# Kernel tuning notes

Measured on AMD Instinct MI355X. Metric: run time of the kernel, lower is better.

## Reference

```python
import jax, jax.numpy as jnp
import numpy as np
from jax import lax

D_MODEL = 1024
D_STATE = 16
D_CONV = 4
EXPAND = 2
D_INNER = D_MODEL * EXPAND
BATCH = 2
SEQLEN = 2048


def setup_inputs() -> dict:
    key = jax.random.key(0)
    ks = jax.random.split(key, 8)
    sc = lambda k, shape, s: jax.random.normal(k, shape, dtype=jnp.float32) * s
    x = jax.random.normal(ks[0], (BATCH, SEQLEN, D_MODEL), dtype=jnp.float32)
    W_in = sc(ks[1], (D_MODEL, 2 * D_INNER), 0.02)          # in_proj (no bias)
    conv_w = sc(ks[2], (D_INNER, 1, D_CONV), 0.1)            # depthwise conv kernel (O, I/g, K)
    conv_b = jnp.zeros((D_INNER,), jnp.float32)
    W_param = sc(ks[3], (D_INNER, 1 + 2 * D_STATE), 0.02)    # param_proj (no bias)
    w_dt = sc(ks[4], (D_INNER,), 0.1)                        # dt_proj weight (d_inner, 1) flattened
    b_dt = jnp.zeros((D_INNER,), jnp.float32)
    A_log = jnp.log(jnp.tile(jnp.arange(1, D_STATE + 1, dtype=jnp.float32), (D_INNER, 1)))
    D_param = jnp.ones((D_INNER,), jnp.float32)
    W_out = sc(ks[5], (D_INNER, D_MODEL), 0.02)              # out_proj (no bias)
    return {"x": x, "W_in": W_in, "conv_w": conv_w, "conv_b": conv_b,
            "W_param": W_param, "w_dt": w_dt, "b_dt": b_dt,
            "A_log": A_log, "D_param": D_param, "W_out": W_out}


def _silu(v):
    return v * jax.nn.sigmoid(v)


def _forward(x, W_in, conv_w, conv_b, W_param, w_dt, b_dt, A_log, D_param, W_out):
    # input projection -> two branches
    xz = x @ W_in                                   # (B, S, 2*d_inner)
    x_branch, z_branch = jnp.split(xz, 2, axis=-1)
    # depthwise causal conv1d (torch pads k-1 both sides then slices [:seqlen] == left pad k-1)
    xc = lax.conv_general_dilated(
        x_branch.transpose(0, 2, 1), conv_w,
        window_strides=(1,), padding=[(D_CONV - 1, 0)],
        feature_group_count=D_INNER,
        dimension_numbers=("NCH", "OIH", "NCH"))
    x_branch = _silu((xc + conv_b[None, :, None]).transpose(0, 2, 1))  # (B, S, d_inner)
    # SSM parameters
    params = x_branch @ W_param                     # (B, S, 1+2n)
    dt_raw = params[..., :1]                        # (B, S, 1)
    B_mat = params[..., 1:1 + D_STATE]              # (B, S, n)
    C_mat = params[..., 1 + D_STATE:]               # (B, S, n)
    dt = jax.nn.softplus(dt_raw * w_dt + b_dt)      # (B, S, d_inner)
    A = -jnp.exp(A_log)                             # (d_inner, n)

    def step(h, inp):
        x_t, dt_t, B_t, C_t = inp                   # (B,i),(B,i),(B,n),(B,n)
        A_bar = jnp.exp(A * dt_t[..., None])        # (B, i, n)
        h = A_bar * h + (dt_t[..., None] * B_t[:, None, :]) * x_t[..., None]
        y_t = jnp.einsum('bin,bn->bi', h, C_t)
        return h, y_t

    h0 = jnp.zeros((x.shape[0], D_INNER, D_STATE), x.dtype)
    xs = (x_branch.transpose(1, 0, 2), dt.transpose(1, 0, 2),
          B_mat.transpose(1, 0, 2), C_mat.transpose(1, 0, 2))
    _, ys = lax.scan(step, h0, xs)                  # ys: (S, B, d_inner)
    y = ys.transpose(1, 0, 2) + D_param * x_branch
    y = y * _silu(z_branch)
    return y @ W_out                                # (B, S, d_model)


def reference(x, W_in, conv_w, conv_b, W_param, w_dt, b_dt, A_log, D_param, W_out):
    return _forward(x, W_in, conv_w, conv_b, W_param, w_dt, b_dt, A_log, D_param, W_out)
```

## Files before the change

### kernel.cpp

```cpp
#include <hip/hip_runtime.h>

typedef unsigned int uint;
typedef unsigned short ushort;

using f32x4  = __attribute__((ext_vector_type(4))) float;
using bf16x8 = __attribute__((ext_vector_type(8))) short;

#define LOG2E 1.44269504f
#define LN2   0.69314718f

__device__ __forceinline__ float fexp2(float x) { return __builtin_amdgcn_exp2f(x); }
__device__ __forceinline__ float flog2(float x) { return __builtin_amdgcn_logf(x); }
__device__ __forceinline__ float frcp (float x) { return __builtin_amdgcn_rcpf(x); }
__device__ __forceinline__ float fsilu(float x) {
  return x * frcp(1.f + fexp2(-LOG2E * x));
}
__device__ __forceinline__ float fsoftplus(float u) {
  float e = fexp2(u * LOG2E);
  float l = LN2 * flog2(1.f + e);
  return (u > 20.f) ? u : l;
}

__device__ __forceinline__ ushort f2b(float f) {
  uint u = __builtin_bit_cast(uint, f);
  u = (u + 0x7fffu + ((u >> 16) & 1u)) >> 16;
  return (ushort)u;
}
__device__ __forceinline__ float b2f(ushort h) {
  return __builtin_bit_cast(float, (uint)h << 16);
}

__device__ __forceinline__ void gload_lds16(const void* g, void* l) {
  __builtin_amdgcn_global_load_lds(
      (const __attribute__((address_space(1))) uint*)g,
      (__attribute__((address_space(3))) uint*)l, 16, 0, 0);
}

#define SBAR  asm volatile("s_barrier" ::: "memory")
#define LG0   do { asm volatile("s_waitcnt lgkmcnt(0)" ::: "memory"); \
                   __builtin_amdgcn_sched_barrier(0); } while (0)
#define VMW(n) do { asm volatile("s_waitcnt vmcnt(" #n ")" ::: "memory"); \
                    __builtin_amdgcn_sched_barrier(0); } while (0)

__global__ __launch_bounds__(256) void cvt_bf16(const float* __restrict__ in,
                                                ushort* __restrict__ out) {
  const int idx = blockIdx.x * 256 + threadIdx.x;
  const float4 v = *(const float4*)&in[(size_t)idx << 2];
  ushort4 o = { f2b(v.x), f2b(v.y), f2b(v.z), f2b(v.w) };
  *(ushort4*)&out[(size_t)idx << 2] = o;
}

__global__ __launch_bounds__(256) void transpose_cvt(const float* __restrict__ in,
                                                     ushort* __restrict__ out,
                                                     int R, int C) {
  __shared__ float tile[32][33];
  const int c0 = blockIdx.x << 5, r0 = blockIdx.y << 5;
  const int tx = threadIdx.x, ty = threadIdx.y;
  for (int j = ty; j < 32; j += 8)
    tile[j][tx] = in[(size_t)(r0 + j) * C + c0 + tx];
  __syncthreads();
  for (int j = ty; j < 32; j += 8)
    out[(size_t)(c0 + j) * R + r0 + tx] = f2b(tile[tx][j]);
}

__global__ __launch_bounds__(256) void wprep(const float* __restrict__ Wp,
                                             ushort* __restrict__ whi,
                                             ushort* __restrict__ wlo) {
  const int idx = blockIdx.x * 256 + threadIdx.x;
  const int n = idx >> 11, k = idx & 2047;
  float v = (n < 33) ? Wp[k * 33 + n] : 0.f;
  ushort h = f2b(v);
  whi[idx] = h;
  wlo[idx] = f2b(v - b2f(h));
}

__device__ __forceinline__ void ldfA(bf16x8 (&a)[8], const ushort* base,
                                     int wq, int lane) {
  const int fr = lane & 15;
  const int ce = (((lane >> 4) ^ (fr & 7)) << 3);
  #pragma unroll
  for (int mi = 0; mi < 4; ++mi) {
    const ushort* p = base + (wq + mi * 16 + fr) * 64;
    a[mi * 2 + 0] = *(const bf16x8*)(p + ce);
    a[mi * 2 + 1] = *(const bf16x8*)(p + (ce ^ 32));
  }
}
__device__ __forceinline__ void ldfB(bf16x8 (&b)[4], const ushort* base,
                                     int wq, int lane) {
  const int fr = lane & 15;
  const int ce = (((lane >> 4) ^ (fr & 7)) << 3);
  #pragma unroll
  for (int ni = 0; ni < 2; ++ni) {
    const ushort* p = base + (wq + ni * 16 + fr) * 64;
    b[ni * 2 + 0] = *(const bf16x8*)(p + ce);
    b[ni * 2 + 1] = *(const bf16x8*)(p + (ce ^ 32));
  }
}
__device__ __forceinline__ void mfma16(f32x4 (&acc)[8][4], const bf16x8 (&a)[8],
                                       const bf16x8 (&b)[4], int qm, int qn) {
  #pragma unroll
  for (int mi = 0; mi < 4; ++mi)
    #pragma unroll
    for (int ni = 0; ni < 2; ++ni)
      #pragma unroll
      for (int s = 0; s < 2; ++s)
        acc[qm * 4 + mi][qn * 2 + ni] = __builtin_amdgcn_mfma_f32_16x16x32_bf16(
            a[mi * 2 + s], b[ni * 2 + s], acc[qm * 4 + mi][qn * 2 + ni], 0, 0, 0);
}

__global__ __launch_bounds__(512, 2) void gemm_bf16_8ph(
    const ushort* __restrict__ A, const ushort* __restrict__ Bt,
    float* __restrict__ C, int M, int N, int K, int lgx) {
  __shared__ __align__(16) ushort lds[65536];
  const int tid = threadIdx.x;
  int w = blockIdx.x;
  const int chunk = (int)(gridDim.x >> 3);
  w = (w & 7) * chunk + (w >> 3);
  const int m0 = (w >> lgx) << 8;
  const int n0 = (w & ((1 << lgx) - 1)) << 8;
  const int lane = tid & 63, wid = tid >> 6;
  const int wm = wid >> 2, wn = wid & 3;
  const int srow = tid >> 3;
  const int scol = (((tid & 7) ^ (srow & 7)) << 3);
  const int swave = wid << 9;

  auto stA = [&](int t, int h) {
    const ushort* g = A + (size_t)(m0 + h * 128 + srow) * K + (t << 6) + scol;
    ushort* l = lds + ((t & 1) << 14) + (h << 13) + swave;
    gload_lds16(g, l);
    gload_lds16(g + (size_t)64 * K, l + 4096);
  };
  auto stB = [&](int t, int h) {
    const ushort* g = Bt + (size_t)(n0 + h * 128 + srow) * K + (t << 6) + scol;
    ushort* l = lds + 32768 + ((t & 1) << 14) + (h << 13) + swave;
    gload_lds16(g, l);
    gload_lds16(g + (size_t)64 * K, l + 4096);
  };

  f32x4 acc[8][4] = {};
  const int niter = K >> 7;

  stA(0, 0); stB(0, 0); stA(0, 1); stB(0, 1); stA(1, 0);
  VMW(2);
  SBAR;

  for (int it = 0; it < niter; ++it) {
    const int E = it << 1, O = E | 1;
    const bool pred = (it < niter - 1);
    const ushort* A0 = lds;
    const ushort* B0 = lds + 32768;
    const ushort* A1 = lds + 16384;
    const ushort* B1 = lds + 49152;
    bf16x8 a[8], b0[4], b1[4];
    ldfA(a, A0, wm * 128, lane);
    ldfB(b0, B0, wn * 64, lane);
    stB(O, 0);
    SBAR; LG0;
    __builtin_amdgcn_s_setprio(1); mfma16(acc, a, b0, 0, 0);
    __builtin_amdgcn_sched_barrier(0); __builtin_amdgcn_s_setprio(0);
    SBAR;
    ldfB(b1, B0, wn * 64 + 32, lane);
    stA(O, 1);
    SBAR; LG0;
    __builtin_amdgcn_s_setprio(1); mfma16(acc, a, b1, 0, 1);
    __builtin_amdgcn_sched_barrier(0); __builtin_amdgcn_s_setprio(0);
    SBAR;
    ldfA(a, A0, wm * 128 + 64, lane);
    stB(O, 1);
    SBAR; LG0;
    __builtin_amdgcn_s_setprio(1); mfma16(acc, a, b0, 1, 0);
    __builtin_amdgcn_sched_barrier(0); __builtin_amdgcn_s_setprio(0);
    SBAR;
    if (pred) stA(E + 2, 0);
    SBAR; LG0;
    __builtin_amdgcn_s_setprio(1); mfma16(acc, a, b1, 1, 1);
    __builtin_amdgcn_sched_barrier(0); __builtin_amdgcn_s_setprio(0);
    if (pred) { VMW(2); } else { VMW(0); }
    SBAR;
    ldfA(a, A1, wm * 128, lane);
    ldfB(b0, B1, wn * 64, lane);
    if (pred) stB(E + 2, 0);
    SBAR; LG0;
    __builtin_amdgcn_s_setprio(1); mfma16(acc, a, b0, 0, 0);
    __builtin_amdgcn_sched_barrier(0); __builtin_amdgcn_s_setprio(0);
    SBAR;
    ldfB(b1, B1, wn * 64 + 32, lane);
    if (pred) stA(E + 2, 1);
    SBAR; LG0;
    __builtin_amdgcn_s_setprio(1); mfma16(acc, a, b1, 0, 1);
    __builtin_amdgcn_sched_barrier(0); __builtin_amdgcn_s_setprio(0);
    SBAR;
    ldfA(a, A1, wm * 128 + 64, lane);
    if (pred) stB(E + 2, 1);
    SBAR; LG0;
    __builtin_amdgcn_s_setprio(1); mfma16(acc, a, b0, 1, 0);
    __builtin_amdgcn_sched_barrier(0); __builtin_amdgcn_s_setprio(0);
    SBAR;
    if (pred) stA(O + 2, 0);
    SBAR; LG0;
    __builtin_amdgcn_s_setprio(1); mfma16(acc, a, b1, 1, 1);
    __builtin_amdgcn_sched_barrier(0); __builtin_amdgcn_s_setprio(0);
    VMW(2);
    SBAR;
  }

  const int rbase = m0 + wm * 128 + ((lane >> 4) << 2);
  const int cbase = n0 + wn * 64 + (lane & 15);
  #pragma unroll
  for (int mi = 0; mi < 8; ++mi)
    #pragma unroll
    for (int ni = 0; ni < 4; ++ni)
      #pragma unroll
      for (int r = 0; r < 4; ++r)
        C[(size_t)(rbase + mi * 16 + r) * N + cbase + ni * 16] = acc[mi][ni][r];
}

__global__ __launch_bounds__(256) void gemm_bf16(const ushort* __restrict__ A,
                                                 const ushort* __restrict__ Bt,
                                                 float* __restrict__ C,
                                                 int M, int N, int K, int lgx) {
  __shared__ __align__(16) ushort As[128 * 64];
  __shared__ __align__(16) ushort Bs[128 * 64];
  const int tid  = threadIdx.x;
  int w = (blockIdx.y << lgx) + blockIdx.x;
  const int chunk = (int)((gridDim.x * gridDim.y) >> 3);
  w = (w & 7) * chunk + (w >> 3);
  const int m0 = (w >> lgx) << 7, n0 = (w & ((1 << lgx) - 1)) << 7;
  const int lane = tid & 63, wid = tid >> 6;
  const int wm   = wid >> 1, wn = wid & 1;
  const int fr   = lane & 15;
  const int kg   = (lane >> 4) << 3;
  const int g_row = tid >> 3;
  const int g_col = (tid & 7) << 3;
  f32x4 acc[4][4] = {};
  for (int k0 = 0; k0 < K; k0 += 64) {
    __syncthreads();
    const ushort* gA = A  + (size_t)(m0 + g_row) * K + k0 + g_col;
    const ushort* gB = Bt + (size_t)(n0 + g_row) * K + k0 + g_col;
    #pragma unroll
    for (int j = 0; j < 4; ++j) {
      gload_lds16(gA + (size_t)(j * 32) * K, As + j * 2048 + wid * 512);
      gload_lds16(gB + (size_t)(j * 32) * K, Bs + j * 2048 + wid * 512);
    }
    __syncthreads();
    #pragma unroll
    for (int ks = 0; ks < 64; ks += 32) {
      bf16x8 a[4], b[4];
      #pragma unroll
      for (int m = 0; m < 4; ++m)
        a[m] = *(const bf16x8*)(As + (wm * 64 + m * 16 + fr) * 64 + ks + kg);
      #pragma unroll
      for (int n = 0; n < 4; ++n)
        b[n] = *(const bf16x8*)(Bs + (wn * 64 + n * 16 + fr) * 64 + ks + kg);
      #pragma unroll
      for (int m = 0; m < 4; ++m)
        #pragma unroll
        for (int n = 0; n < 4; ++n)
          acc[m][n] = __builtin_amdgcn_mfma_f32_16x16x32_bf16(a[m], b[n], acc[m][n], 0, 0, 0);
    }
  }
  const int rbase = m0 + wm * 64 + ((lane >> 4) << 2);
  const int cbase = n0 + wn * 64 + fr;
  #pragma unroll
  for (int sm = 0; sm < 4; ++sm)
    #pragma unroll
    for (int sn = 0; sn < 4; ++sn)
      #pragma unroll
      for (int r = 0; r < 4; ++r)
        C[(size_t)(rbase + sm * 16 + r) * N + cbase + sn * 16] = acc[sm][sn][r];
}

__global__ __launch_bounds__(256) void params_mfma(const ushort* __restrict__ xhi,
                                                   const ushort* __restrict__ xlo,
                                                   const ushort* __restrict__ whi,
                                                   const ushort* __restrict__ wlo,
                                                   float* __restrict__ xz) {
  __shared__ __align__(16) ushort Ah[128 * 64], Al[128 * 64];
  __shared__ __align__(16) ushort Bh[64 * 64],  Bl[64 * 64];
  const int mt = blockIdx.x >> 2, ks = blockIdx.x & 3;
  const int m0 = mt << 7;
  const int k00 = ks << 9;
  const int tid = threadIdx.x, lane = tid & 63, wid = tid >> 6;
  const int fr = lane & 15, kg = (lane >> 4) << 3;
  const int g_row = tid >> 3, g_col = (tid & 7) << 3;
  f32x4 acc[2][4] = {};
  for (int k0 = k00; k0 < k00 + 512; k0 += 64) {
    __syncthreads();
    const ushort* gAh = xhi + (size_t)(m0 + g_row) * 2048 + k0 + g_col;
    const ushort* gAl = xlo + (size_t)(m0 + g_row) * 2048 + k0 + g_col;
    #pragma unroll
    for (int j = 0; j < 4; ++j) {
      gload_lds16(gAh + (size_t)(j * 32) * 2048, Ah + j * 2048 + wid * 512);
      gload_lds16(gAl + (size_t)(j * 32) * 2048, Al + j * 2048 + wid * 512);
    }
    const ushort* gWh = whi + (size_t)g_row * 2048 + k0 + g_col;
    const ushort* gWl = wlo + (size_t)g_row * 2048 + k0 + g_col;
    gload_lds16(gWh, Bh + wid * 512);
    gload_lds16(gWh + (size_t)32 * 2048, Bh + 2048 + wid * 512);
    gload_lds16(gWl, Bl + wid * 512);
    gload_lds16(gWl + (size_t)32 * 2048, Bl + 2048 + wid * 512);
    __syncthreads();
    #pragma unroll
    for (int kss = 0; kss < 64; kss += 32) {
      bf16x8 ah[2], al[2], bh[4], bl[4];
      #pragma unroll
      for (int m = 0; m < 2; ++m) {
        ah[m] = *(const bf16x8*)(Ah + (wid * 32 + m * 16 + fr) * 64 + kss + kg);
        al[m] = *(const bf16x8*)(Al + (wid * 32 + m * 16 + fr) * 64 + kss + kg);
      }
      #pragma unroll
      for (int n = 0; n < 4; ++n) {
        bh[n] = *(const bf16x8*)(Bh + (n * 16 + fr) * 64 + kss + kg);
        bl[n] = *(const bf16x8*)(Bl + (n * 16 + fr) * 64 + kss + kg);
      }
      #pragma unroll
      for (int m = 0; m < 2; ++m)
        #pragma unroll
        for (int n = 0; n < 4; ++n) {
          acc[m][n] = __builtin_amdgcn_mfma_f32_16x16x32_bf16(ah[m], bh[n], acc[m][n], 0, 0, 0);
          acc[m][n] = __builtin_amdgcn_mfma_f32_16x16x32_bf16(ah[m], bl[n], acc[m][n], 0, 0, 0);
          acc[m][n] = __builtin_amdgcn_mfma_f32_16x16x32_bf16(al[m], bh[n], acc[m][n], 0, 0, 0);
        }
    }
  }
  const int rbase = m0 + wid * 32 + ((lane >> 4) << 2);
  #pragma unroll
  for (int m = 0; m < 2; ++m)
    #pragma unroll
    for (int n = 0; n < 4; ++n)
      #pragma unroll
      for (int r = 0; r < 4; ++r)
        xz[(size_t)(rbase + m * 16 + r) * 4096 + (ks << 6) + n * 16 + fr] = acc[m][n][r];
}

__global__ __launch_bounds__(256) void conv_silu(const float* __restrict__ xz,
                                                 const float* __restrict__ cw,
                                                 const float* __restrict__ cb,
                                                 float* __restrict__ xs,
                                                 ushort* __restrict__ xhi,
                                                 ushort* __restrict__ xlo) {
  const int idx = blockIdx.x * 256 + threadIdx.x;
  const int c4  = (idx & 511) << 2;
  const int row = idx >> 9;
  const int t   = row & 2047;
  float acc[4], w0[4], w1[4], w2[4], w3[4];
  *(float4*)acc = *(const float4*)&cb[c4];
  *(float4*)w0 = *(const float4*)&cw[(c4 + 0) << 2];
  *(float4*)w1 = *(const float4*)&cw[(c4 + 1) << 2];
  *(float4*)w2 = *(const float4*)&cw[(c4 + 2) << 2];
  *(float4*)w3 = *(const float4*)&cw[(c4 + 3) << 2];
  #pragma unroll
  for (int k = 0; k < 4; ++k) {
    if (t - 3 + k >= 0) {
      const float4 v = *(const float4*)&xz[(size_t)(row - 3 + k) * 4096 + c4];
      acc[0] = fmaf(w0[k], v.x, acc[0]);
      acc[1] = fmaf(w1[k], v.y, acc[1]);
      acc[2] = fmaf(w2[k], v.z, acc[2]);
      acc[3] = fmaf(w3[k], v.w, acc[3]);
    }
  }
  float o[4];
  ushort hi[4], lo[4];
  #pragma unroll
  for (int j = 0; j < 4; ++j) {
    o[j]  = fsilu(acc[j]);
    hi[j] = f2b(o[j]);
    lo[j] = f2b(o[j] - b2f(hi[j]));
  }
  *(float4*) &xs [(size_t)idx << 2] = *(float4*)o;
  *(ushort4*)&xhi[(size_t)idx << 2] = *(ushort4*)hi;
  *(ushort4*)&xlo[(size_t)idx << 2] = *(ushort4*)lo;
}

__global__ __launch_bounds__(256) void scan_pass1(const float* __restrict__ xs,
                                                  const float* __restrict__ xz,
                                                  const float* __restrict__ w_dt,
                                                  const float* __restrict__ b_dt,
                                                  const float* __restrict__ A_log,
                                                  float2* __restrict__ sums) {
  const int blk = blockIdx.x;
  const int c   = blk & 63, bg = blk >> 6;
  const int b   = bg >> 3, cg = bg & 7;
  const int tid = threadIdx.x;
  const int i   = (cg << 8) + tid;
  __shared__ float bc_l[32][32];
  __shared__ float dtr_l[32];
  const size_t row0 = (size_t)b * 2048 + c * 32;
  for (int idx = tid; idx < 1024; idx += 256) {
    int t = idx >> 5, n = idx & 31;
    const float* p = xz + (row0 + t) * 4096 + 1 + n;
    bc_l[t][n] = (p[0] + p[64]) + (p[128] + p[192]);
  }
  if (tid < 32) {
    const float* p = xz + (row0 + tid) * 4096;
    dtr_l[tid] = (p[0] + p[64]) + (p[128] + p[192]);
  }
  const float w = w_dt[i], bb = b_dt[i];
  float An2[16];
  {
    const float4* al = (const float4*)&A_log[(size_t)i * 16];
    #pragma unroll
    for (int q = 0; q < 4; ++q) {
      float4 v = al[q];
      An2[4 * q + 0] = -fexp2(v.x * LOG2E) * LOG2E;
      An2[4 * q + 1] = -fexp2(v.y * LOG2E) * LOG2E;
      An2[4 * q + 2] = -fexp2(v.z * LOG2E) * LOG2E;
      An2[4 * q + 3] = -fexp2(v.w * LOG2E) * LOG2E;
    }
  }
  float h[16] = {};
  float dts = 0.f;
  __syncthreads();
  const float* xcol = xs + row0 * 2048 + i;
  #pragma unroll 4
  for (int t = 0; t < 32; ++t) {
    float dt = fsoftplus(fmaf(dtr_l[t], w, bb));
    dts += dt;
    float dtx = dt * xcol[(size_t)t * 2048];
    const f32x4* bp = (const f32x4*)&bc_l[t][0];
    #pragma unroll
    for (int q = 0; q < 4; ++q) {
      f32x4 Bv = bp[q];
      #pragma unroll
      for (int j = 0; j < 4; ++j) {
        const int n = 4 * q + j;
        float Ab = fexp2(An2[n] * dt);
        h[n] = fmaf(Ab, h[n], dtx * Bv[j]);
      }
    }
  }
  float4* sp = (float4*)(sums + ((size_t)(b * 64 + c) << 15) + (size_t)i * 16);
  #pragma unroll
  for (int q = 0; q < 8; ++q)
    sp[q] = make_float4(fexp2(An2[2 * q] * dts), h[2 * q],
                        fexp2(An2[2 * q + 1] * dts), h[2 * q + 1]);
}

__global__ __launch_bounds__(256) void scan_mid(float2* __restrict__ sums) {
  const int g = blockIdx.x * 256 + threadIdx.x;
  const int b = g >> 15, r = g & 32767;
  float2* base = sums + ((size_t)b << 21) + r;
  float h = 0.f;
  #pragma unroll
  for (int cb = 0; cb < 64; cb += 16) {
    float2 s[16];
    #pragma unroll
    for (int j = 0; j < 16; ++j) s[j] = base[(size_t)(cb + j) << 15];
    #pragma unroll
    for (int j = 0; j < 16; ++j) {
      base[(size_t)(cb + j) << 15].x = h;
      h = fmaf(s[j].x, h, s[j].y);
    }
  }
}

__global__ __launch_bounds__(256) void scan_pass2(const float* __restrict__ xs,
                                                  const float* __restrict__ xz,
                                                  const float* __restrict__ w_dt,
                                                  const float* __restrict__ b_dt,
                                                  const float* __restrict__ A_log,
                                                  const float* __restrict__ D_param,
                                                  const float2* __restrict__ sums,
                                                  ushort* __restrict__ yg) {
  const int blk = blockIdx.x;
  const int c   = blk & 63, bg = blk >> 6;
  const int b   = bg >> 3, cg = bg & 7;
  const int tid = threadIdx.x;
  const int i   = (cg << 8) + tid;
  __shared__ float bc_l[32][32];
  __shared__ float dtr_l[32];
  const size_t row0 = (size_t)b * 2048 + c * 32;
  for (int idx = tid; idx < 1024; idx += 256) {
    int t = idx >> 5, n = idx & 31;
    const float* p = xz + (row0 + t) * 4096 + 1 + n;
    bc_l[t][n] = (p[0] + p[64]) + (p[128] + p[192]);
  }
  if (tid < 32) {
    const float* p = xz + (row0 + tid) * 4096;
    dtr_l[tid] = (p[0] + p[64]) + (p[128] + p[192]);
  }
  const float w = w_dt[i], bb = b_dt[i];
  const float Dp = D_param[i];
  float An2[16];
  {
    const float4* al = (const float4*)&A_log[(size_t)i * 16];
    #pragma unroll
    for (int q = 0; q < 4; ++q) {
      float4 v = al[q];
      An2[4 * q + 0] = -fexp2(v.x * LOG2E) * LOG2E;
      An2[4 * q + 1] = -fexp2(v.y * LOG2E) * LOG2E;
      An2[4 * q + 2] = -fexp2(v.z * LOG2E) * LOG2E;
      An2[4 * q + 3] = -fexp2(v.w * LOG2E) * LOG2E;
    }
  }
  float h[16];
  {
    const float4* sp = (const float4*)(sums + ((size_t)(b * 64 + c) << 15) + (size_t)i * 16);
    #pragma unroll
    for (int q = 0; q < 8; ++q) {
      float4 v = sp[q];
      h[2 * q]     = v.x;
      h[2 * q + 1] = v.z;
    }
  }
  __syncthreads();
  const float*  xcol = xs + row0 * 2048 + i;
  const float*  zcol = xz + row0 * 4096 + 2048 + i;
  ushort*       ocol = yg + row0 * 2048 + i;
  #pragma unroll 4
  for (int t = 0; t < 32; ++t) {
    float dt = fsoftplus(fmaf(dtr_l[t], w, bb));
    float xv = xcol[(size_t)t * 2048];
    float dtx = dt * xv;
    float y = Dp * xv;
    const f32x4* bp = (const f32x4*)&bc_l[t][0];
    const f32x4* cp = (const f32x4*)&bc_l[t][16];
    #pragma unroll
    for (int q = 0; q < 4; ++q) {
      f32x4 Bv = bp[q], Cv = cp[q];
      #pragma unroll
      for (int j = 0; j < 4; ++j) {
        const int n = 4 * q + j;
        float Ab = fexp2(An2[n] * dt);
        h[n] = fmaf(Ab, h[n], dtx * Bv[j]);
        y = fmaf(h[n], Cv[j], y);
      }
    }
    float z = zcol[(size_t)t * 4096];
    ocol[(size_t)t * 2048] = f2b(y * fsilu(z));
  }
}

extern "C" void kernel_launch(void* const* d_in, const int* in_sizes, int n_in,
                              void* d_out, int out_size, void* d_ws, size_t ws_size,
                              hipStream_t stream) {
  const float* x       = (const float*)d_in[0];
  const float* W_in    = (const float*)d_in[1];
  const float* conv_w  = (const float*)d_in[2];
  const float* conv_b  = (const float*)d_in[3];
  const float* W_param = (const float*)d_in[4];
  const float* w_dt    = (const float*)d_in[5];
  const float* b_dt    = (const float*)d_in[6];
  const float* A_log   = (const float*)d_in[7];
  const float* D_param = (const float*)d_in[8];
  const float* W_out   = (const float*)d_in[9];
  float* out = (float*)d_out;

  char* ws = (char*)d_ws;
  float*  xz     = (float*) (ws);
  float*  x_s    = (float*) (ws + 67108864);
  ushort* WpT_hi = (ushort*)(ws + 100663296);
  ushort* WpT_lo = (ushort*)(ws + 100925440);
  float2* sums   = (float2*)(ws + 101203968);
  ushort* x_hi   = (ushort*)(ws + 101203968);
  ushort* x_lo   = (ushort*)(ws + 117981184);
  ushort* WoutT  = (ushort*)(ws + 134758400);
  ushort* yg     = (ushort*)(ws + 138952704);
  ushort* xA     = (ushort*)(ws + 155729920);
  ushort* WinT   = (ushort*)(ws + 164118528);

  cvt_bf16<<<4096, 256, 0, stream>>>(x, xA);
  transpose_cvt<<<dim3(128, 32), dim3(32, 8), 0, stream>>>(W_in,  WinT,  1024, 4096);
  transpose_cvt<<<dim3(32, 64),  dim3(32, 8), 0, stream>>>(W_out, WoutT, 2048, 1024);
  wprep<<<512, 256, 0, stream>>>(W_param, WpT_hi, WpT_lo);
  gemm_bf16_8ph<<<256, 512, 0, stream>>>(xA, WinT, xz, 4096, 4096, 1024, 4);
  conv_silu<<<8192, 256, 0, stream>>>(xz, conv_w, conv_b, x_s, x_hi, x_lo);
  params_mfma<<<128, 256, 0, stream>>>(x_hi, x_lo, WpT_hi, WpT_lo, xz);
  scan_pass1<<<1024, 256, 0, stream>>>(x_s, xz, w_dt, b_dt, A_log, sums);
  scan_mid<<<256, 256, 0, stream>>>(sums);
  scan_pass2<<<1024, 256, 0, stream>>>(x_s, xz, w_dt, b_dt, A_log, D_param, sums, yg);
  gemm_bf16<<<dim3(8, 32), 256, 0, stream>>>(yg, WoutT, out, 4096, 1024, 2048, 3);
}
```

Measured before the change: 232.8 us.

## Split scan chunk sums into SoA arrays and retile out-proj GEMM to 64x128

```diff
diff --git a/kernel.cpp b/kernel.cpp
--- a/kernel.cpp
+++ b/kernel.cpp
@@ -215,59 +215,56 @@
         C[(size_t)(rbase + mi * 16 + r) * N + cbase + ni * 16] = acc[mi][ni][r];
 }
 
-__global__ __launch_bounds__(256) void gemm_bf16(const ushort* __restrict__ A,
-                                                 const ushort* __restrict__ Bt,
-                                                 float* __restrict__ C,
-                                                 int M, int N, int K, int lgx) {
-  __shared__ __align__(16) ushort As[128 * 64];
+__global__ __launch_bounds__(256) void gemm_bf16_64x128(
+    const ushort* __restrict__ A, const ushort* __restrict__ Bt,
+    float* __restrict__ C, int M, int N, int K, int lgx) {
+  __shared__ __align__(16) ushort As[64 * 64];
   __shared__ __align__(16) ushort Bs[128 * 64];
-  const int tid  = threadIdx.x;
-  int w = (blockIdx.y << lgx) + blockIdx.x;
-  const int chunk = (int)((gridDim.x * gridDim.y) >> 3);
+  const int tid = threadIdx.x;
+  int w = blockIdx.x;
+  const int chunk = (int)(gridDim.x >> 3);
   w = (w & 7) * chunk + (w >> 3);
-  const int m0 = (w >> lgx) << 7, n0 = (w & ((1 << lgx) - 1)) << 7;
+  const int m0 = (w >> lgx) << 6;
+  const int n0 = (w & ((1 << lgx) - 1)) << 7;
   const int lane = tid & 63, wid = tid >> 6;
-  const int wm   = wid >> 1, wn = wid & 1;
-  const int fr   = lane & 15;
-  const int kg   = (lane >> 4) << 3;
-  const int g_row = tid >> 3;
-  const int g_col = (tid & 7) << 3;
-  f32x4 acc[4][4] = {};
+  const int fr = lane & 15, kg = (lane >> 4) << 3;
+  const int g_row = tid >> 3, g_col = (tid & 7) << 3;
+  f32x4 acc[4][2] = {};
   for (int k0 = 0; k0 < K; k0 += 64) {
     __syncthreads();
     const ushort* gA = A  + (size_t)(m0 + g_row) * K + k0 + g_col;
     const ushort* gB = Bt + (size_t)(n0 + g_row) * K + k0 + g_col;
-    #pragma unroll
-    for (int j = 0; j < 4; ++j) {
-      gload_lds16(gA + (size_t)(j * 32) * K, As + j * 2048 + wid * 512);
+    gload_lds16(gA,                   As + wid * 512);
+    gload_lds16(gA + (size_t)32 * K,  As + 2048 + wid * 512);
+    #pragma unroll
+    for (int j = 0; j < 4; ++j)
       gload_lds16(gB + (size_t)(j * 32) * K, Bs + j * 2048 + wid * 512);
-    }
     __syncthreads();
     #pragma unroll
     for (int ks = 0; ks < 64; ks += 32) {
-      bf16x8 a[4], b[4];
+      bf16x8 a[4], b[2];
       #pragma unroll
       for (int m = 0; m < 4; ++m)
-        a[m] = *(const bf16x8*)(As + (wm * 64 + m * 16 + fr) * 64 + ks + kg);
-      #pragma unroll
-      for (int n = 0; n < 4; ++n)
-        b[n] = *(const bf16x8*)(Bs + (wn * 64 + n * 16 + fr) * 64 + ks + kg);
+        a[m] = *(const bf16x8*)(As + (m * 16 + fr) * 64 + ks + kg);
+      #pragma unroll
+      for (int n = 0; n < 2; ++n)
+        b[n] = *(const bf16x8*)(Bs + (wid * 32 + n * 16 + fr) * 64 + ks + kg);
       #pragma unroll
       for (int m = 0; m < 4; ++m)
         #pragma unroll
-        for (int n = 0; n < 4; ++n)
+        for (int n = 0; n < 2; ++n)
           acc[m][n] = __builtin_amdgcn_mfma_f32_16x16x32_bf16(a[m], b[n], acc[m][n], 0, 0, 0);
     }
   }
-  const int rbase = m0 + wm * 64 + ((lane >> 4) << 2);
-  const int cbase = n0 + wn * 64 + fr;
-  #pragma unroll
-  for (int sm = 0; sm < 4; ++sm)
-    #pragma unroll
-    for (int sn = 0; sn < 4; ++sn)
+  const int rbase = m0 + ((lane >> 4) << 2);
+  const int cbase = n0 + wid * 32 + fr;
+  #pragma unroll
+  for (int mi = 0; mi < 4; ++mi)
+    #pragma unroll
+    for (int ni = 0; ni < 2; ++ni)
       #pragma unroll
       for (int r = 0; r < 4; ++r)
-        C[(size_t)(rbase + sm * 16 + r) * N + cbase + sn * 16] = acc[sm][sn][r];
+        C[(size_t)(rbase + mi * 16 + r) * N + cbase + ni * 16] = acc[mi][ni][r];
 }
 
 __global__ __launch_bounds__(256) void params_mfma(const ushort* __restrict__ xhi,
@@ -377,7 +374,8 @@
                                                   const float* __restrict__ w_dt,
                                                   const float* __restrict__ b_dt,
                                                   const float* __restrict__ A_log,
-                                                  float2* __restrict__ sums) {
+                                                  float* __restrict__ sums_ap,
+                                                  float* __restrict__ sums_h) {
   const int blk = blockIdx.x;
   const int c   = blk & 63, bg = blk >> 6;
   const int b   = bg >> 3, cg = bg & 7;
@@ -429,27 +427,36 @@
       }
     }
   }
-  float4* sp = (float4*)(sums + ((size_t)(b * 64 + c) << 15) + (size_t)i * 16);
-  #pragma unroll
-  for (int q = 0; q < 8; ++q)
-    sp[q] = make_float4(fexp2(An2[2 * q] * dts), h[2 * q],
-                        fexp2(An2[2 * q + 1] * dts), h[2 * q + 1]);
-}
-
-__global__ __launch_bounds__(256) void scan_mid(float2* __restrict__ sums) {
+  const size_t sb = ((size_t)(b * 64 + c) << 15) + (size_t)i * 16;
+  #pragma unroll
+  for (int q = 0; q < 4; ++q) {
+    f32x4 av = { fexp2(An2[4 * q + 0] * dts), fexp2(An2[4 * q + 1] * dts),
+                 fexp2(An2[4 * q + 2] * dts), fexp2(An2[4 * q + 3] * dts) };
+    f32x4 hv = { h[4 * q + 0], h[4 * q + 1], h[4 * q + 2], h[4 * q + 3] };
+    *(f32x4*)&sums_ap[sb + q * 4] = av;
+    *(f32x4*)&sums_h [sb + q * 4] = hv;
+  }
+}
+
+__global__ __launch_bounds__(256) void scan_mid(float* __restrict__ sums_ap,
+                                                const float* __restrict__ sums_h) {
   const int g = blockIdx.x * 256 + threadIdx.x;
   const int b = g >> 15, r = g & 32767;
-  float2* base = sums + ((size_t)b << 21) + r;
+  float* ba = sums_ap + ((size_t)b << 21) + r;
+  const float* bh = sums_h + ((size_t)b << 21) + r;
   float h = 0.f;
   #pragma unroll
   for (int cb = 0; cb < 64; cb += 16) {
-    float2 s[16];
-    #pragma unroll
-    for (int j = 0; j < 16; ++j) s[j] = base[(size_t)(cb + j) << 15];
+    float a16[16], h16[16];
     #pragma unroll
     for (int j = 0; j < 16; ++j) {
-      base[(size_t)(cb + j) << 15].x = h;
-      h = fmaf(s[j].x, h, s[j].y);
+      a16[j] = ba[(size_t)(cb + j) << 15];
+      h16[j] = bh[(size_t)(cb + j) << 15];
+    }
+    #pragma unroll
+    for (int j = 0; j < 16; ++j) {
+      ba[(size_t)(cb + j) << 15] = h;
+      h = fmaf(a16[j], h, h16[j]);
     }
   }
 }
@@ -460,7 +467,7 @@
                                                   const float* __restrict__ b_dt,
                                                   const float* __restrict__ A_log,
                                                   const float* __restrict__ D_param,
-                                                  const float2* __restrict__ sums,
+                                                  const float* __restrict__ sums_ap,
                                                   ushort* __restrict__ yg) {
   const int blk = blockIdx.x;
   const int c   = blk & 63, bg = blk >> 6;
@@ -495,12 +502,14 @@
   }
   float h[16];
   {
-    const float4* sp = (const float4*)(sums + ((size_t)(b * 64 + c) << 15) + (size_t)i * 16);
-    #pragma unroll
-    for (int q = 0; q < 8; ++q) {
-      float4 v = sp[q];
-      h[2 * q]     = v.x;
-      h[2 * q + 1] = v.z;
+    const float4* spa = (const float4*)(sums_ap + ((size_t)(b * 64 + c) << 15) + (size_t)i * 16);
+    #pragma unroll
+    for (int q = 0; q < 4; ++q) {
+      float4 v = spa[q];
+      h[4 * q + 0] = v.x;
+      h[4 * q + 1] = v.y;
+      h[4 * q + 2] = v.z;
+      h[4 * q + 3] = v.w;
     }
   }
   __syncthreads();
@@ -547,17 +556,18 @@
   float* out = (float*)d_out;
 
   char* ws = (char*)d_ws;
-  float*  xz     = (float*) (ws);
-  float*  x_s    = (float*) (ws + 67108864);
-  ushort* WpT_hi = (ushort*)(ws + 100663296);
-  ushort* WpT_lo = (ushort*)(ws + 100925440);
-  float2* sums   = (float2*)(ws + 101203968);
-  ushort* x_hi   = (ushort*)(ws + 101203968);
-  ushort* x_lo   = (ushort*)(ws + 117981184);
-  ushort* WoutT  = (ushort*)(ws + 134758400);
-  ushort* yg     = (ushort*)(ws + 138952704);
-  ushort* xA     = (ushort*)(ws + 155729920);
-  ushort* WinT   = (ushort*)(ws + 164118528);
+  float*  xz      = (float*) (ws);
+  float*  x_s     = (float*) (ws + 67108864);
+  ushort* WpT_hi  = (ushort*)(ws + 100663296);
+  ushort* WpT_lo  = (ushort*)(ws + 100925440);
+  float*  sums_ap = (float*) (ws + 101203968);
+  float*  sums_h  = (float*) (ws + 117981184);
+  ushort* x_hi    = (ushort*)(ws + 101203968);
+  ushort* x_lo    = (ushort*)(ws + 117981184);
+  ushort* WoutT   = (ushort*)(ws + 134758400);
+  ushort* yg      = (ushort*)(ws + 138952704);
+  ushort* xA      = (ushort*)(ws + 155729920);
+  ushort* WinT    = (ushort*)(ws + 164118528);
 
   cvt_bf16<<<4096, 256, 0, stream>>>(x, xA);
   transpose_cvt<<<dim3(128, 32), dim3(32, 8), 0, stream>>>(W_in,  WinT,  1024, 4096);
@@ -566,8 +576,8 @@
   gemm_bf16_8ph<<<256, 512, 0, stream>>>(xA, WinT, xz, 4096, 4096, 1024, 4);
   conv_silu<<<8192, 256, 0, stream>>>(xz, conv_w, conv_b, x_s, x_hi, x_lo);
   params_mfma<<<128, 256, 0, stream>>>(x_hi, x_lo, WpT_hi, WpT_lo, xz);
-  scan_pass1<<<1024, 256, 0, stream>>>(x_s, xz, w_dt, b_dt, A_log, sums);
-  scan_mid<<<256, 256, 0, stream>>>(sums);
-  scan_pass2<<<1024, 256, 0, stream>>>(x_s, xz, w_dt, b_dt, A_log, D_param, sums, yg);
-  gemm_bf16<<<dim3(8, 32), 256, 0, stream>>>(yg, WoutT, out, 4096, 1024, 2048, 3);
-}
+  scan_pass1<<<1024, 256, 0, stream>>>(x_s, xz, w_dt, b_dt, A_log, sums_ap, sums_h);
+  scan_mid<<<256, 256, 0, stream>>>(sums_ap, sums_h);
+  scan_pass2<<<1024, 256, 0, stream>>>(x_s, xz, w_dt, b_dt, A_log, D_param, sums_ap, yg);
+  gemm_bf16_64x128<<<512, 256, 0, stream>>>(yg, WoutT, out, 4096, 1024, 2048, 3);
+}
```

Result: faster. 223.9 us (-3.8%).
